# Optimization experiments

Measured on AMD Instinct MI355X. Metric: run time of the kernel, lower is better.

Reference implementation:

```python
import jax, jax.numpy as jnp
import numpy as np
from jax.scipy.special import erf

N = 100000
PATCH = 10           # cells per dim: covers 2*nsigma*sigma_max / spacing <= 9
SPACING = (0.5, 0.5, 0.5)
NSIGMA = 3.0


def setup_inputs() -> dict:
    key = jax.random.key(0)
    k1, k2, k3, k4 = jax.random.split(key, 4)
    # sigma in [0.25, 0.75] distance units = [0.5, 1.5] x grid spacing
    sigma = 0.25 + 0.5 * jax.random.uniform(k1, (N, 3), dtype=jnp.float32)
    time = jax.random.uniform(k2, (N,), dtype=jnp.float32) * 10.0
    charge = jax.random.uniform(k3, (N,), dtype=jnp.float32) * 1000.0
    tail = jax.random.normal(k4, (N, 3), dtype=jnp.float32) * 20.0
    grid_spacing = jnp.asarray(SPACING, dtype=jnp.float32)
    nsigma = jnp.asarray(NSIGMA, dtype=jnp.float32)
    return {"sigma": sigma, "time": time, "charge": charge, "tail": tail,
            "grid_spacing": grid_spacing, "nsigma": nsigma}


def _transform(point, time):
    # pdims=(1,2), tdim=-1: new = [point[:,1], point[:,2], time]
    return jnp.stack([point[:, 1], point[:, 2], time], axis=-1)


def _raster_depos(grid_spacing, center, sigma, charge, nsigma):
    # center, sigma: [N,3]; returns rasters [N,P,P,P], offsets [N,3] int32
    imin = jnp.floor((center - nsigma * sigma) / grid_spacing)   # [N,3]
    offsets = imin.astype(jnp.int32)
    k = jnp.arange(PATCH + 1, dtype=center.dtype)                # cell edges index
    edges = (imin[:, :, None] + k) * grid_spacing[None, :, None]  # [N,3,P+1]
    z = (edges - center[:, :, None]) / (jnp.sqrt(2.0).astype(center.dtype) * sigma[:, :, None])
    cdf = 0.5 * (1.0 + erf(z))                                   # [N,3,P+1]
    w = cdf[..., 1:] - cdf[..., :-1]                             # [N,3,P] per-dim cell integrals
    rasters = (charge[:, None, None, None]
               * w[:, 0, :, None, None]
               * w[:, 1, None, :, None]
               * w[:, 2, None, None, :])                         # [N,P,P,P]
    return rasters, offsets


def reference(sigma, time, charge, tail, grid_spacing, nsigma):
    center = _transform(tail, time)
    rasters, offsets = _raster_depos(grid_spacing, center, sigma, charge, nsigma)
    return rasters, offsets
```

## Files before the change

kernel.cpp:

```cpp
#include <hip/hip_runtime.h>
#include <hip/hip_bf16.h>

#define CELLS 1000
#define DPB   50
#define NTH   256

__global__ __launch_bounds__(NTH) void raster_kernel(
    const float* __restrict__ sigma,
    const float* __restrict__ time,
    const float* __restrict__ charge,
    const float* __restrict__ tail,
    const float* __restrict__ gs,
    const float* __restrict__ nsig,
    float* __restrict__ out_r,
    float* __restrict__ out_off,
    int n)
{
    const int d0  = blockIdx.x * DPB;
    const int tid = threadIdx.x;

    __shared__ float wq[DPB][32];

#pragma unroll
    for (int idx = tid; idx < DPB * 30; idx += NTH) {
        const int d   = idx / 30;
        const int r   = idx - d * 30;
        const int dim = r / 10;
        const int k   = r - dim * 10;
        const int depo = d0 + d;
        if (depo < n) {
            float c;
            if (dim == 0)      c = tail[depo * 3 + 1];
            else if (dim == 1) c = tail[depo * 3 + 2];
            else               c = time[depo];
            const float sg = sigma[depo * 3 + dim];
            const float sp = gs[dim];
            const float ns = nsig[0];
            const float imin = floorf((c - ns * sg) / sp);
            const float inv  = 1.0f / (1.41421356237309f * sg);
            const float e0   = (imin + (float)k) * sp;
            const float cdf0 = 0.5f * (1.0f + erff((e0 - c) * inv));
            const float cdf1 = 0.5f * (1.0f + erff((e0 + sp - c) * inv));
            wq[d][dim * 10 + k] = cdf1 - cdf0;
            if (k == 0) {
                out_off[(size_t)depo * 3 + dim] = (float)(int)imin;
                if (dim == 0) wq[d][30] = charge[depo];
            }
        }
    }
    __syncthreads();

    if (tid < 250) {
        const int c4 = tid;
        int a0[4], a1[4], a2[4];
#pragma unroll
        for (int c = 0; c < 4; ++c) {
            const int cell = c4 * 4 + c;
            a0[c] = cell / 100;
            a1[c] = 10 + (cell / 10) % 10;
            a2[c] = 20 + cell % 10;
        }

        for (int d = 0; d < DPB; ++d) {
            const int depo = d0 + d;
            if (depo < n) {
                const float q = wq[d][30];
                float4 v;
                v.x = q * wq[d][a0[0]] * wq[d][a1[0]] * wq[d][a2[0]];
                v.y = q * wq[d][a0[1]] * wq[d][a1[1]] * wq[d][a2[1]];
                v.z = q * wq[d][a0[2]] * wq[d][a1[2]] * wq[d][a2[2]];
                v.w = q * wq[d][a0[3]] * wq[d][a1[3]] * wq[d][a2[3]];
                float4* dst = reinterpret_cast<float4*>(out_r + (size_t)depo * CELLS) + c4;
                *dst = v;
            }
        }
    }
}

extern "C" void kernel_launch(void* const* d_in, const int* in_sizes, int n_in,
                              void* d_out, int out_size, void* d_ws, size_t ws_size,
                              hipStream_t stream) {
    const float* sigma  = (const float*)d_in[0];
    const float* time_  = (const float*)d_in[1];
    const float* charge = (const float*)d_in[2];
    const float* tail   = (const float*)d_in[3];
    const float* gs     = (const float*)d_in[4];
    const float* nsig   = (const float*)d_in[5];

    const int n = in_sizes[1];

    float* out_r   = (float*)d_out;
    float* out_off = (float*)d_out + (size_t)n * CELLS;

    const int grid = (n + DPB - 1) / DPB;
    raster_kernel<<<grid, NTH, 0, stream>>>(sigma, time_, charge, tail, gs, nsig,
                                            out_r, out_off, n);
}
```

Baseline: 88.60 us.

## Assign depo pairs per wavefront with persistent grid-stride loop, dropping block barrier

Restructures the kernel so each 64-lane wavefront computes the per-dimension weights for two deposits and then writes their 2x1000 raster cells itself, looping over pairs in a grid-stride fashion with a capped grid. This removes the block-wide __syncthreads and the serial 50-depo loop per block, and lets weight computation and stores of different waves overlap. It relies on wavefront-level lockstep for LDS visibility without an explicit barrier, which is a correctness risk. Index math for cell lookups is now recomputed inline.

```diff
diff --git a/kernel.cpp b/kernel.cpp
--- a/kernel.cpp
+++ b/kernel.cpp
@@ -2,8 +2,9 @@
 #include <hip/hip_bf16.h>
 
 #define CELLS 1000
-#define DPB   50
 #define NTH   256
+#define WPB   4
+#define NBLK  2048
 
 __global__ __launch_bounds__(NTH) void raster_kernel(
     const float* __restrict__ sigma,
@@ -16,62 +17,87 @@
     float* __restrict__ out_off,
     int n)
 {
-    const int d0  = blockIdx.x * DPB;
-    const int tid = threadIdx.x;
+    const int tid  = threadIdx.x;
+    const int lane = tid & 63;
+    const int wv   = tid >> 6;
 
-    __shared__ float wq[DPB][32];
+    __shared__ float wq[WPB][2][32];
+
+    const bool cp  = (lane < 60);
+    const int  cd  = lane / 30;
+    const int  r   = cp ? (lane - cd * 30) : 0;
+    const int  dim = r / 10;
+    const int  k   = r - dim * 10;
+
+    const float ns = nsig[0];
+    const float sp = gs[cp ? dim : 0];
+
+    const int npairs  = (n + 1) >> 1;
+    const int stride  = gridDim.x * WPB;
+    int p = blockIdx.x * WPB + wv;
+
+    for (; p < npairs; p += stride) {
+        const int d0 = p * 2;
+
+        if (cp) {
+            const int depo = d0 + cd;
+            if (depo < n) {
+                float c;
+                if (dim == 0)      c = tail[depo * 3 + 1];
+                else if (dim == 1) c = tail[depo * 3 + 2];
+                else               c = time[depo];
+                const float sg   = sigma[depo * 3 + dim];
+                const float imin = floorf((c - ns * sg) / sp);
+                const float inv  = 1.0f / (1.41421356237309f * sg);
+                const float e0   = (imin + (float)k) * sp;
+                const float cdf0 = 0.5f * (1.0f + erff((e0 - c) * inv));
+                const float cdf1 = 0.5f * (1.0f + erff((e0 + sp - c) * inv));
+                wq[wv][cd][dim * 10 + k] = cdf1 - cdf0;
+                if (k == 0) {
+                    out_off[(size_t)depo * 3 + dim] = (float)(int)imin;
+                    if (dim == 0) wq[wv][cd][30] = charge[depo];
+                }
+            }
+        }
 
 #pragma unroll
-    for (int idx = tid; idx < DPB * 30; idx += NTH) {
-        const int d   = idx / 30;
-        const int r   = idx - d * 30;
-        const int dim = r / 10;
-        const int k   = r - dim * 10;
-        const int depo = d0 + d;
-        if (depo < n) {
-            float c;
-            if (dim == 0)      c = tail[depo * 3 + 1];
-            else if (dim == 1) c = tail[depo * 3 + 2];
-            else               c = time[depo];
-            const float sg = sigma[depo * 3 + dim];
-            const float sp = gs[dim];
-            const float ns = nsig[0];
-            const float imin = floorf((c - ns * sg) / sp);
-            const float inv  = 1.0f / (1.41421356237309f * sg);
-            const float e0   = (imin + (float)k) * sp;
-            const float cdf0 = 0.5f * (1.0f + erff((e0 - c) * inv));
-            const float cdf1 = 0.5f * (1.0f + erff((e0 + sp - c) * inv));
-            wq[d][dim * 10 + k] = cdf1 - cdf0;
-            if (k == 0) {
-                out_off[(size_t)depo * 3 + dim] = (float)(int)imin;
-                if (dim == 0) wq[d][30] = charge[depo];
-            }
-        }
-    }
-    __syncthreads();
-
-    if (tid < 250) {
-        const int c4 = tid;
-        int a0[4], a1[4], a2[4];
-#pragma unroll
-        for (int c = 0; c < 4; ++c) {
-            const int cell = c4 * 4 + c;
-            a0[c] = cell / 100;
-            a1[c] = 10 + (cell / 10) % 10;
-            a2[c] = 20 + cell % 10;
-        }
-
-        for (int d = 0; d < DPB; ++d) {
-            const int depo = d0 + d;
-            if (depo < n) {
-                const float q = wq[d][30];
-                float4 v;
-                v.x = q * wq[d][a0[0]] * wq[d][a1[0]] * wq[d][a2[0]];
-                v.y = q * wq[d][a0[1]] * wq[d][a1[1]] * wq[d][a2[1]];
-                v.z = q * wq[d][a0[2]] * wq[d][a1[2]] * wq[d][a2[2]];
-                v.w = q * wq[d][a0[3]] * wq[d][a1[3]] * wq[d][a2[3]];
-                float4* dst = reinterpret_cast<float4*>(out_r + (size_t)depo * CELLS) + c4;
-                *dst = v;
+        for (int s = 0; s < 8; ++s) {
+            const int idx = s * 64 + lane;
+            if (idx < 500) {
+                const int dd   = idx / 250;
+                const int c4   = idx - dd * 250;
+                const int depo = d0 + dd;
+                if (depo < n) {
+                    const float q = wq[wv][dd][30];
+                    float4 v;
+                    {
+                        const int cell = c4 * 4 + 0;
+                        v.x = q * wq[wv][dd][cell / 100]
+                                * wq[wv][dd][10 + (cell / 10) % 10]
+                                * wq[wv][dd][20 + cell % 10];
+                    }
+                    {
+                        const int cell = c4 * 4 + 1;
+                        v.y = q * wq[wv][dd][cell / 100]
+                                * wq[wv][dd][10 + (cell / 10) % 10]
+                                * wq[wv][dd][20 + cell % 10];
+                    }
+                    {
+                        const int cell = c4 * 4 + 2;
+                        v.z = q * wq[wv][dd][cell / 100]
+                                * wq[wv][dd][10 + (cell / 10) % 10]
+                                * wq[wv][dd][20 + cell % 10];
+                    }
+                    {
+                        const int cell = c4 * 4 + 3;
+                        v.w = q * wq[wv][dd][cell / 100]
+                                * wq[wv][dd][10 + (cell / 10) % 10]
+                                * wq[wv][dd][20 + cell % 10];
+                    }
+                    float4* dst =
+                        reinterpret_cast<float4*>(out_r + (size_t)depo * CELLS) + c4;
+                    *dst = v;
+                }
             }
         }
     }
@@ -92,7 +118,9 @@
     float* out_r   = (float*)d_out;
     float* out_off = (float*)d_out + (size_t)n * CELLS;
 
-    const int grid = (n + DPB - 1) / DPB;
+    const int npairs = (n + 1) >> 1;
+    int grid = (npairs + WPB - 1) / WPB;
+    if (grid > NBLK) grid = NBLK;
     raster_kernel<<<grid, NTH, 0, stream>>>(sigma, time_, charge, tail, gs, nsig,
                                             out_r, out_off, n);
 }
```

Measured after the change: 82.99 us. -6.3%, faster.

## Flatten output write loop across all threads and shrink deposits per block

Applied to the files above, without the earlier changes.

Replaces the per-deposit loop, in which only 250 of 256 threads wrote one float4 per deposit, with a flat loop over all float4s in the block's contiguous output region. Threads now cover consecutive addresses across deposits with full utilization. Block size goes to 512 threads and deposits per block drop to 32, which gives more blocks and fewer serial iterations. Index math (divisions by 250 and 10) is now done per element, adding some integer arithmetic.

```diff
diff --git a/kernel.cpp b/kernel.cpp
--- a/kernel.cpp
+++ b/kernel.cpp
@@ -2,8 +2,9 @@
 #include <hip/hip_bf16.h>
 
 #define CELLS 1000
-#define DPB   50
-#define NTH   256
+#define DPB   32
+#define NTH   512
+#define F4PB  8000
 
 __global__ __launch_bounds__(NTH) void raster_kernel(
     const float* __restrict__ sigma,
@@ -33,9 +34,9 @@
             if (dim == 0)      c = tail[depo * 3 + 1];
             else if (dim == 1) c = tail[depo * 3 + 2];
             else               c = time[depo];
-            const float sg = sigma[depo * 3 + dim];
-            const float sp = gs[dim];
-            const float ns = nsig[0];
+            const float sg   = sigma[depo * 3 + dim];
+            const float sp   = gs[dim];
+            const float ns   = nsig[0];
             const float imin = floorf((c - ns * sg) / sp);
             const float inv  = 1.0f / (1.41421356237309f * sg);
             const float e0   = (imin + (float)k) * sp;
@@ -50,29 +51,44 @@
     }
     __syncthreads();
 
-    if (tid < 250) {
-        const int c4 = tid;
-        int a0[4], a1[4], a2[4];
+    int valid = (n - d0) * 250;
+    if (valid > F4PB) valid = F4PB;
+
+    float4* const dstbase = reinterpret_cast<float4*>(out_r) + (size_t)blockIdx.x * F4PB;
+
 #pragma unroll
-        for (int c = 0; c < 4; ++c) {
-            const int cell = c4 * 4 + c;
-            a0[c] = cell / 100;
-            a1[c] = 10 + (cell / 10) % 10;
-            a2[c] = 20 + cell % 10;
-        }
+    for (int i = 0; i < 16; ++i) {
+        const int j = i * NTH + tid;
+        if (j < valid) {
+            const int d    = j / 250;
+            const int c4   = j - d * 250;
+            const int cell0 = c4 * 4;
+            const int a0   = cell0 / 100;
+            const float q   = wq[d][30];
+            const float w0q = q * wq[d][a0];
 
-        for (int d = 0; d < DPB; ++d) {
-            const int depo = d0 + d;
-            if (depo < n) {
-                const float q = wq[d][30];
-                float4 v;
-                v.x = q * wq[d][a0[0]] * wq[d][a1[0]] * wq[d][a2[0]];
-                v.y = q * wq[d][a0[1]] * wq[d][a1[1]] * wq[d][a2[1]];
-                v.z = q * wq[d][a0[2]] * wq[d][a1[2]] * wq[d][a2[2]];
-                v.w = q * wq[d][a0[3]] * wq[d][a1[3]] * wq[d][a2[3]];
-                float4* dst = reinterpret_cast<float4*>(out_r + (size_t)depo * CELLS) + c4;
-                *dst = v;
+            float4 v;
+            {
+                const int cell = cell0 + 0;
+                const int t10  = cell / 10;
+                v.x = w0q * wq[d][10 + (t10 - 10 * a0)] * wq[d][20 + (cell - 10 * t10)];
             }
+            {
+                const int cell = cell0 + 1;
+                const int t10  = cell / 10;
+                v.y = w0q * wq[d][10 + (t10 - 10 * a0)] * wq[d][20 + (cell - 10 * t10)];
+            }
+            {
+                const int cell = cell0 + 2;
+                const int t10  = cell / 10;
+                v.z = w0q * wq[d][10 + (t10 - 10 * a0)] * wq[d][20 + (cell - 10 * t10)];
+            }
+            {
+                const int cell = cell0 + 3;
+                const int t10  = cell / 10;
+                v.w = w0q * wq[d][10 + (t10 - 10 * a0)] * wq[d][20 + (cell - 10 * t10)];
+            }
+            dstbase[j] = v;
         }
     }
 }
```

Result: faster. 85.49 us (-3.5%).
